# Optimization experiments

Hardware: AMD Instinct MI355X
Metric: run time of the kernel (lower is better)

## Reference

```python
import jax, jax.numpy as jnp
import numpy as np

KS = 3          # deformable kernel size
PAD = 1         # zero padding
N = KS * KS     # sample points per pixel


def conv2d(x, w, b=None, padding=1):
    out = jax.lax.conv_general_dilated(
        x, w, (1, 1), [(padding, padding)] * 2,
        dimension_numbers=('NCHW', 'OIHW', 'NCHW'))
    if b is not None:
        out = out + b[None, :, None, None]
    return out


def setup_inputs() -> dict:
    key = jax.random.key(0)
    k0, k1, k2, k3 = jax.random.split(key, 4)
    B, C, H, W, O = 4, 64, 128, 128, 64
    x = jax.random.normal(k0, (B, C, H, W), jnp.float32)
    # p_conv / m_conv are zero-init in the original; use small random weights
    # so offsets/modulation are non-trivial but sampling stays local.
    w_p = jax.random.normal(k1, (2 * N, C, 3, 3), jnp.float32) * 0.01
    b_p = jnp.zeros((2 * N,), jnp.float32)
    w_m = jax.random.normal(k2, (N, C, 3, 3), jnp.float32) * 0.01
    b_m = jnp.zeros((N,), jnp.float32)
    w_conv = jax.random.normal(k3, (O, C, KS, KS), jnp.float32) / np.sqrt(C * N)
    return {'x': x, 'w_p': w_p, 'b_p': b_p, 'w_m': w_m, 'b_m': b_m, 'w_conv': w_conv}


def reference(x, w_p, b_p, w_m, b_m, w_conv):
    B, C, H, W = x.shape
    offset = conv2d(x, w_p, b_p)              # (B, 2N, H, W): first N rows(x), last N cols(y)
    m = jax.nn.sigmoid(conv2d(x, w_m, b_m))   # (B, N, H, W) modulation
    xp = jnp.pad(x, ((0, 0), (0, 0), (PAD, PAD), (PAD, PAD)))  # zero_padding
    Hp, Wp = H + 2 * PAD, W + 2 * PAD

    # p = p_0 + p_n + offset  (coords in padded image, p_0 starts at 1)
    r = (KS - 1) // 2
    pn_x, pn_y = jnp.meshgrid(jnp.arange(-r, r + 1), jnp.arange(-r, r + 1), indexing='ij')
    pn = jnp.concatenate([pn_x.reshape(-1), pn_y.reshape(-1)]).astype(x.dtype)          # (2N,)
    p0_x, p0_y = jnp.meshgrid(jnp.arange(1, H + 1), jnp.arange(1, W + 1), indexing='ij')
    p0 = jnp.concatenate([jnp.tile(p0_x[None], (N, 1, 1)),
                          jnp.tile(p0_y[None], (N, 1, 1))], 0).astype(x.dtype)           # (2N,H,W)
    p = offset + pn[None, :, None, None] + p0[None]
    p = jnp.moveaxis(p, 1, -1)                # (B,H,W,2N)

    fx = jnp.floor(jax.lax.stop_gradient(p[..., :N]))  # p.detach().floor()
    fy = jnp.floor(jax.lax.stop_gradient(p[..., N:]))
    q_lt_x = jnp.clip(fx, 0, Hp - 1).astype(jnp.int32)
    q_lt_y = jnp.clip(fy, 0, Wp - 1).astype(jnp.int32)
    q_rb_x = jnp.clip(fx + 1, 0, Hp - 1).astype(jnp.int32)
    q_rb_y = jnp.clip(fy + 1, 0, Wp - 1).astype(jnp.int32)
    px = jnp.clip(p[..., :N], 0, Hp - 1)
    py = jnp.clip(p[..., N:], 0, Wp - 1)

    # bilinear kernel weights (same algebra as torch version)
    g_lt = (1 + (q_lt_x - px)) * (1 + (q_lt_y - py))
    g_rb = (1 - (q_rb_x - px)) * (1 - (q_rb_y - py))
    g_lb = (1 + (q_lt_x - px)) * (1 - (q_rb_y - py))
    g_rt = (1 - (q_rb_x - px)) * (1 + (q_lt_y - py))

    xf = xp.reshape(B, C, Hp * Wp)

    def gather(qx, qy):
        idx = (qx * Wp + qy).reshape(B, 1, -1)                      # (B,1,H*W*N)
        return jnp.take_along_axis(xf, idx, axis=2).reshape(B, C, H, W, N)

    x_off = (g_lt[:, None] * gather(q_lt_x, q_lt_y)
             + g_rb[:, None] * gather(q_rb_x, q_rb_y)
             + g_lb[:, None] * gather(q_lt_x, q_rb_y)
             + g_rt[:, None] * gather(q_rb_x, q_lt_y))               # (B,C,H,W,N)

    x_off = x_off * jnp.moveaxis(m, 1, -1)[:, None]                  # modulation (DCNv2)

    # _reshape_x_offset + conv(kernel=ks, stride=ks) == einsum over the N samples
    out = jnp.einsum('bchwk,ock->bohw', x_off,
                     w_conv.reshape(w_conv.shape[0], C, N))
    return out
```

## Files before the change

### kernel.cpp

```cpp
#include <hip/hip_runtime.h>
#include <hip/hip_bf16.h>

#define BB 4
#define CC 64
#define HH 128
#define WW 128
#define OO 64
#define NN 9
#define HW 16384
#define HP 130
#define WP 130

#define WPMB_F  0
#define BPM_OFF 9216
#define WCB_F   9248
#define XT_F    27680
#define PX_OFF  2124832
#define PSZ     589824

typedef __attribute__((ext_vector_type(8))) short s8v;
typedef __attribute__((ext_vector_type(8))) unsigned short u8v;
typedef __attribute__((ext_vector_type(4))) float f4v;

__device__ __forceinline__ unsigned short f2bu(float f) {
    unsigned int b = __float_as_uint(f);
    return (unsigned short)((b + 0x7FFFu + ((b >> 16) & 1u)) >> 16);
}
__device__ __forceinline__ float bu2f(unsigned short u) {
    return __uint_as_float(((unsigned int)u) << 16);
}

__global__ void __launch_bounds__(256) k_pxt(const float* __restrict__ x,
                                             const float* __restrict__ wp,
                                             const float* __restrict__ bp,
                                             const float* __restrict__ wm,
                                             const float* __restrict__ bm,
                                             const float* __restrict__ wcv,
                                             float* __restrict__ ws) {
    __shared__ unsigned short tile[64][66];
    int blk = blockIdx.x;
    int t = threadIdx.x;
    if (blk >= 1024) {
        int tid = (blk - 1024) * 256 + t;
        if (tid < 18432) {
            int r = tid / 576;
            int kk = tid % 576;
            int kt = kk >> 6;
            int c = kk & 63;
            int dy = kt / 3, dx = kt % 3;
            float v = 0.f;
            if (r < 18)       v = wp[((r * 64 + c) * 3 + dy) * 3 + dx];
            else if (r < 27)  v = wm[(((r - 18) * 64 + c) * 3 + dy) * 3 + dx];
            ((unsigned short*)(ws + WPMB_F))[tid] = f2bu(v);
        } else if (tid < 18459) {
            int i = tid - 18432;
            ws[BPM_OFF + i] = (i < 18) ? bp[i] : bm[i - 18];
        } else if (tid >= 20480) {
            int d = tid - 20480;
            int o = d / 576;
            int kk = d % 576;
            int kt = kk >> 6;
            int c = kk & 63;
            ((unsigned short*)(ws + WCB_F))[o * 576 + kk] = f2bu(wcv[(o * 64 + c) * 9 + kt]);
        }
        return;
    }
    int b = blk >> 8;
    int hw0 = (blk & 255) * 64;
    unsigned short* xt = (unsigned short*)(ws + XT_F);
#pragma unroll
    for (int p = 0; p < 16; p++) {
        int c = p * 4 + (t >> 6);
        int i = t & 63;
        tile[c][i] = f2bu(x[((size_t)(b * 64 + c)) * HW + hw0 + i]);
    }
    __syncthreads();
#pragma unroll
    for (int p = 0; p < 16; p++) {
        int i = p * 4 + (t >> 6);
        int c = t & 63;
        xt[((size_t)(b * HW + hw0 + i)) * 64 + c] = tile[c][i];
    }
}

__global__ void __launch_bounds__(256) k_off(const float* __restrict__ ws,
                                             float* __restrict__ wsout) {
    __shared__ unsigned short Awld[2][32 * 72];
    __shared__ unsigned short Bld[2][64 * 72];

    int t = threadIdx.x;
    int lane = t & 63;
    int wid = t >> 6;
    int ln15 = lane & 15;
    int quad = lane >> 4;

    int blk = blockIdx.x;
    int b = blk >> 8;
    int hw0 = (blk & 255) * 64;

    const unsigned short* wpmb = (const unsigned short*)(ws + WPMB_F);
    const unsigned short* xtb = (const unsigned short*)(ws + XT_F) + (size_t)b * HW * 64;
    const float* bpm = ws + BPM_OFF;

    int aq_row = t >> 3, aq_g = t & 7;
    int bq_pix = t & 63, bq_half = t >> 6;
    int ph = (hw0 + bq_pix) >> 7;
    int pw = (hw0 + bq_pix) & 127;

    f4v acc[2];
    acc[0] = (f4v){0.f, 0.f, 0.f, 0.f};
    acc[1] = (f4v){0.f, 0.f, 0.f, 0.f};

    const u8v z = (u8v){0, 0, 0, 0, 0, 0, 0, 0};

    {
        u8v av = *(const u8v*)(wpmb + aq_row * 576 + aq_g * 8);
        int h2 = ph - 1, w2 = pw - 1;
        bool val = ((unsigned)h2 < 128u) && ((unsigned)w2 < 128u);
        u8v e0 = z, e1 = z;
        if (val) {
            const unsigned short* src = xtb + ((size_t)(h2 * 128 + w2)) * 64 + bq_half * 16;
            e0 = *(const u8v*)(src);
            e1 = *(const u8v*)(src + 8);
        }
        *(u8v*)(&Awld[0][aq_row * 72 + aq_g * 8]) = av;
        *(u8v*)(&Bld[0][bq_pix * 72 + bq_half * 16]) = e0;
        *(u8v*)(&Bld[0][bq_pix * 72 + bq_half * 16 + 8]) = e1;
    }
    __syncthreads();

#pragma unroll 1
    for (int kt = 0; kt < 9; kt++) {
        int cur = kt & 1, nxt = cur ^ 1;
        u8v an = z, n0 = z, n1 = z;
        if (kt < 8) {
            int k2 = kt + 1;
            an = *(const u8v*)(wpmb + aq_row * 576 + k2 * 64 + aq_g * 8);
            int dy = k2 / 3, dx = k2 % 3;
            int h2 = ph + dy - 1, w2 = pw + dx - 1;
            bool val = ((unsigned)h2 < 128u) && ((unsigned)w2 < 128u);
            if (val) {
                const unsigned short* src = xtb + ((size_t)(h2 * 128 + w2)) * 64 + bq_half * 16;
                n0 = *(const u8v*)(src);
                n1 = *(const u8v*)(src + 8);
            }
        }
#pragma unroll
        for (int ks = 0; ks < 2; ks++) {
            s8v bf = *(const s8v*)(&Bld[cur][(wid * 16 + ln15) * 72 + ks * 32 + quad * 8]);
#pragma unroll
            for (int mt = 0; mt < 2; mt++) {
                s8v af = *(const s8v*)(&Awld[cur][(mt * 16 + ln15) * 72 + ks * 32 + quad * 8]);
                acc[mt] = __builtin_amdgcn_mfma_f32_16x16x32_bf16(af, bf, acc[mt], 0, 0, 0);
            }
        }
        if (kt < 8) {
            *(u8v*)(&Awld[nxt][aq_row * 72 + aq_g * 8]) = an;
            *(u8v*)(&Bld[nxt][bq_pix * 72 + bq_half * 16]) = n0;
            *(u8v*)(&Bld[nxt][bq_pix * 72 + bq_half * 16 + 8]) = n1;
        }
        __syncthreads();
    }

    int p = hw0 + wid * 16 + ln15;
    int h = p >> 7, w = p & 127;
    float* pxA = wsout + PX_OFF;
    float* pyA = pxA + PSZ;
    float* mmA = pyA + PSZ;
#pragma unroll
    for (int mt = 0; mt < 2; mt++) {
#pragma unroll
        for (int r = 0; r < 4; r++) {
            int oc = mt * 16 + quad * 4 + r;
            if (oc < 27) {
                float v = acc[mt][r] + bpm[oc];
                if (oc < 9) {
                    int ki = oc / 3;
                    pxA[((size_t)b * NN + oc) * HW + p] = v + (float)(ki - 1) + (float)(h + 1);
                } else if (oc < 18) {
                    int k = oc - 9;
                    int kj = k % 3;
                    pyA[((size_t)b * NN + k) * HW + p] = v + (float)(kj - 1) + (float)(w + 1);
                } else {
                    int k = oc - 18;
                    mmA[((size_t)b * NN + k) * HW + p] = 1.f / (1.f + __expf(-v));
                }
            }
        }
    }
}

__global__ void __launch_bounds__(256) k_gemm(const float* __restrict__ ws,
                                              float* __restrict__ out) {
    __shared__ unsigned short Ald[2][64 * 72];
    __shared__ unsigned short Sld[2][64 * 72];

    int t = threadIdx.x;
    int lane = t & 63;
    int wid = t >> 6;
    int ln15 = lane & 15;
    int quad = lane >> 4;

    int blk = blockIdx.x;
    int b = blk >> 8;
    int hw0 = (blk & 255) * 64;

    const unsigned short* wcb = (const unsigned short*)(ws + WCB_F);
    const unsigned short* xtb = (const unsigned short*)(ws + XT_F) + (size_t)b * HW * 64;
    const float* pxA = ws + PX_OFF;
    const float* pyA = pxA + PSZ;
    const float* mmA = pyA + PSZ;

    int p_loc = t >> 2;
    int cq = t & 3;
    int cbase = cq * 16;
    int arow = t >> 2, ag = t & 3;

    f4v acc[4];
#pragma unroll
    for (int mt = 0; mt < 4; mt++) acc[mt] = (f4v){0.f, 0.f, 0.f, 0.f};

    size_t pbase = (size_t)b * NN * HW + (size_t)(hw0 + p_loc);

    auto desc = [&](float px, float py, float mk,
                    float& g0, float& g1, float& g2, float& g3,
                    int& o0, int& o1, int& o2, int& o3) {
        float fx = floorf(px), fy = floorf(py);
        float pxc = fminf(fmaxf(px, 0.f), (float)(HP - 1));
        float pyc = fminf(fmaxf(py, 0.f), (float)(WP - 1));
        int qltx = (int)fminf(fmaxf(fx, 0.f), (float)(HP - 1));
        int qlty = (int)fminf(fmaxf(fy, 0.f), (float)(WP - 1));
        int qrbx = (int)fminf(fmaxf(fx + 1.f, 0.f), (float)(HP - 1));
        int qrby = (int)fminf(fmaxf(fy + 1.f, 0.f), (float)(WP - 1));

        float gltx = 1.f + ((float)qltx - pxc);
        float glty = 1.f + ((float)qlty - pyc);
        float grbx = 1.f - ((float)qrbx - pxc);
        float grby = 1.f - ((float)qrby - pyc);

        bool vlx = (qltx >= 1) && (qltx <= HH);
        bool vly = (qlty >= 1) && (qlty <= WW);
        bool vrx = (qrbx >= 1) && (qrbx <= HH);
        bool vry = (qrby >= 1) && (qrby <= WW);
        g0 = (vlx && vly) ? gltx * glty * mk : 0.f;
        g1 = (vrx && vry) ? grbx * grby * mk : 0.f;
        g2 = (vlx && vry) ? gltx * grby * mk : 0.f;
        g3 = (vrx && vly) ? grbx * glty * mk : 0.f;

        int xlt = min(max(qltx - 1, 0), HH - 1);
        int ylt = min(max(qlty - 1, 0), WW - 1);
        int xrb = min(max(qrbx - 1, 0), HH - 1);
        int yrb = min(max(qrby - 1, 0), WW - 1);
        o0 = (xlt * WW + ylt) * 64 + cbase;
        o1 = (xrb * WW + yrb) * 64 + cbase;
        o2 = (xlt * WW + yrb) * 64 + cbase;
        o3 = (xrb * WW + ylt) * 64 + cbase;
    };

    float pxn, pyn, mkn;
    {
        float px = pxA[pbase], py = pyA[pbase], mk = mmA[pbase];
        pxn = pxA[pbase + HW]; pyn = pyA[pbase + HW]; mkn = mmA[pbase + HW];
        float g0, g1, g2, g3; int o0, o1, o2, o3;
        desc(px, py, mk, g0, g1, g2, g3, o0, o1, o2, o3);
        u8v e0a = *(const u8v*)(xtb + o0), e0b = *(const u8v*)(xtb + o0 + 8);
        u8v e1a = *(const u8v*)(xtb + o1), e1b = *(const u8v*)(xtb + o1 + 8);
        u8v e2a = *(const u8v*)(xtb + o2), e2b = *(const u8v*)(xtb + o2 + 8);
        u8v e3a = *(const u8v*)(xtb + o3), e3b = *(const u8v*)(xtb + o3 + 8);
        u8v a0 = *(const u8v*)(wcb + arow * 576 + ag * 16);
        u8v a1 = *(const u8v*)(wcb + arow * 576 + ag * 16 + 8);
        u8v sva, svb;
#pragma unroll
        for (int j = 0; j < 8; j++) {
            float va = g0 * bu2f(e0a[j]) + g1 * bu2f(e1a[j])
                     + g2 * bu2f(e2a[j]) + g3 * bu2f(e3a[j]);
            float vb = g0 * bu2f(e0b[j]) + g1 * bu2f(e1b[j])
                     + g2 * bu2f(e2b[j]) + g3 * bu2f(e3b[j]);
            sva[j] = f2bu(va);
            svb[j] = f2bu(vb);
        }
        *(u8v*)(&Sld[0][p_loc * 72 + cbase]) = sva;
        *(u8v*)(&Sld[0][p_loc * 72 + cbase + 8]) = svb;
        *(u8v*)(&Ald[0][arow * 72 + ag * 16]) = a0;
        *(u8v*)(&Ald[0][arow * 72 + ag * 16 + 8]) = a1;
    }
    __syncthreads();

#pragma unroll 1
    for (int kt = 0; kt < 9; kt++) {
        int cur = kt & 1, nxt = cur ^ 1;
        float g0 = 0.f, g1 = 0.f, g2 = 0.f, g3 = 0.f;
        u8v e0a, e0b, e1a, e1b, e2a, e2b, e3a, e3b, a0, a1;
        if (kt < 8) {
            int o0, o1, o2, o3;
            desc(pxn, pyn, mkn, g0, g1, g2, g3, o0, o1, o2, o3);
            e0a = *(const u8v*)(xtb + o0); e0b = *(const u8v*)(xtb + o0 + 8);
            e1a = *(const u8v*)(xtb + o1); e1b = *(const u8v*)(xtb + o1 + 8);
            e2a = *(const u8v*)(xtb + o2); e2b = *(const u8v*)(xtb + o2 + 8);
            e3a = *(const u8v*)(xtb + o3); e3b = *(const u8v*)(xtb + o3 + 8);
            a0 = *(const u8v*)(wcb + arow * 576 + (kt + 1) * 64 + ag * 16);
            a1 = *(const u8v*)(wcb + arow * 576 + (kt + 1) * 64 + ag * 16 + 8);
            if (kt < 7) {
                size_t pn = pbase + (size_t)(kt + 2) * HW;
                pxn = pxA[pn]; pyn = pyA[pn]; mkn = mmA[pn];
            }
        }
#pragma unroll
        for (int ks = 0; ks < 2; ks++) {
            s8v bf = *(const s8v*)(&Sld[cur][(wid * 16 + ln15) * 72 + ks * 32 + quad * 8]);
#pragma unroll
            for (int mt = 0; mt < 4; mt++) {
                s8v af = *(const s8v*)(&Ald[cur][(mt * 16 + ln15) * 72 + ks * 32 + quad * 8]);
                acc[mt] = __builtin_amdgcn_mfma_f32_16x16x32_bf16(af, bf, acc[mt], 0, 0, 0);
            }
        }
        if (kt < 8) {
            u8v sva, svb;
#pragma unroll
            for (int j = 0; j < 8; j++) {
                float va = g0 * bu2f(e0a[j]) + g1 * bu2f(e1a[j])
                         + g2 * bu2f(e2a[j]) + g3 * bu2f(e3a[j]);
                float vb = g0 * bu2f(e0b[j]) + g1 * bu2f(e1b[j])
                         + g2 * bu2f(e2b[j]) + g3 * bu2f(e3b[j]);
                sva[j] = f2bu(va);
                svb[j] = f2bu(vb);
            }
            *(u8v*)(&Sld[nxt][p_loc * 72 + cbase]) = sva;
            *(u8v*)(&Sld[nxt][p_loc * 72 + cbase + 8]) = svb;
            *(u8v*)(&Ald[nxt][arow * 72 + ag * 16]) = a0;
            *(u8v*)(&Ald[nxt][arow * 72 + ag * 16 + 8]) = a1;
        }
        __syncthreads();
    }

    int pix = hw0 + wid * 16 + ln15;
    float* ob = out + (size_t)b * (OO * HW) + pix;
#pragma unroll
    for (int mt = 0; mt < 4; mt++) {
#pragma unroll
        for (int r = 0; r < 4; r++) {
            ob[(size_t)(mt * 16 + quad * 4 + r) * HW] = acc[mt][r];
        }
    }
}

extern "C" void kernel_launch(void* const* d_in, const int* in_sizes, int n_in,
                              void* d_out, int out_size, void* d_ws, size_t ws_size,
                              hipStream_t stream) {
    const float* x   = (const float*)d_in[0];
    const float* wp  = (const float*)d_in[1];
    const float* bp  = (const float*)d_in[2];
    const float* wm  = (const float*)d_in[3];
    const float* bm  = (const float*)d_in[4];
    const float* wcv = (const float*)d_in[5];
    float* ws = (float*)d_ws;
    float* out = (float*)d_out;

    hipLaunchKernelGGL(k_pxt, dim3(1248), dim3(256), 0, stream, x, wp, bp, wm, bm, wcv, ws);
    hipLaunchKernelGGL(k_off, dim3(1024), dim3(256), 0, stream, ws, ws);
    hipLaunchKernelGGL(k_gemm, dim3(1024), dim3(256), 0, stream, ws, out);
}
```

Measured before the change: 116.0 us.

## Fuse offset conv and deformable gemm into one kernel via LDS handoff

Merges the offset/modulation MFMA kernel and the deformable-sampling GEMM kernel into a single kernel. Per-block px/py/mask values now stay in shared memory instead of going through global workspace, which removes one launch and the global write/read of those arrays. Weight fragments (offset-conv and main-conv weights) are also read straight from global/L2 into MFMA operands instead of being staged through LDS, which cuts LDS traffic and usage. In exchange, register pressure rises in the fused kernel and the weight loads now sit on the MFMA critical path.

```diff
diff --git a/kernel.cpp b/kernel.cpp
--- a/kernel.cpp
+++ b/kernel.cpp
@@ -15,8 +15,6 @@
 #define BPM_OFF 9216
 #define WCB_F   9248
 #define XT_F    27680
-#define PX_OFF  2124832
-#define PSZ     589824
 
 typedef __attribute__((ext_vector_type(8))) short s8v;
 typedef __attribute__((ext_vector_type(8))) unsigned short u8v;
@@ -83,10 +81,10 @@
     }
 }
 
-__global__ void __launch_bounds__(256) k_off(const float* __restrict__ ws,
-                                             float* __restrict__ wsout) {
-    __shared__ unsigned short Awld[2][32 * 72];
-    __shared__ unsigned short Bld[2][64 * 72];
+__global__ void __launch_bounds__(256) k_main(const float* __restrict__ ws,
+                                              float* __restrict__ out) {
+    __shared__ unsigned short Sld[2][64 * 72];
+    __shared__ float pxmL[3][NN][64];
 
     int t = threadIdx.x;
     int lane = t & 63;
@@ -99,132 +97,107 @@
     int hw0 = (blk & 255) * 64;
 
     const unsigned short* wpmb = (const unsigned short*)(ws + WPMB_F);
+    const unsigned short* wcb = (const unsigned short*)(ws + WCB_F);
     const unsigned short* xtb = (const unsigned short*)(ws + XT_F) + (size_t)b * HW * 64;
     const float* bpm = ws + BPM_OFF;
 
-    int aq_row = t >> 3, aq_g = t & 7;
-    int bq_pix = t & 63, bq_half = t >> 6;
-    int ph = (hw0 + bq_pix) >> 7;
-    int pw = (hw0 + bq_pix) & 127;
-
-    f4v acc[2];
-    acc[0] = (f4v){0.f, 0.f, 0.f, 0.f};
-    acc[1] = (f4v){0.f, 0.f, 0.f, 0.f};
-
     const u8v z = (u8v){0, 0, 0, 0, 0, 0, 0, 0};
 
     {
-        u8v av = *(const u8v*)(wpmb + aq_row * 576 + aq_g * 8);
-        int h2 = ph - 1, w2 = pw - 1;
-        bool val = ((unsigned)h2 < 128u) && ((unsigned)w2 < 128u);
-        u8v e0 = z, e1 = z;
-        if (val) {
-            const unsigned short* src = xtb + ((size_t)(h2 * 128 + w2)) * 64 + bq_half * 16;
-            e0 = *(const u8v*)(src);
-            e1 = *(const u8v*)(src + 8);
-        }
-        *(u8v*)(&Awld[0][aq_row * 72 + aq_g * 8]) = av;
-        *(u8v*)(&Bld[0][bq_pix * 72 + bq_half * 16]) = e0;
-        *(u8v*)(&Bld[0][bq_pix * 72 + bq_half * 16 + 8]) = e1;
-    }
-    __syncthreads();
-
-#pragma unroll 1
-    for (int kt = 0; kt < 9; kt++) {
-        int cur = kt & 1, nxt = cur ^ 1;
-        u8v an = z, n0 = z, n1 = z;
-        if (kt < 8) {
-            int k2 = kt + 1;
-            an = *(const u8v*)(wpmb + aq_row * 576 + k2 * 64 + aq_g * 8);
-            int dy = k2 / 3, dx = k2 % 3;
-            int h2 = ph + dy - 1, w2 = pw + dx - 1;
+        int bq_pix = t & 63, bq_half = t >> 6;
+        int ph = (hw0 + bq_pix) >> 7;
+        int pw = (hw0 + bq_pix) & 127;
+
+        f4v acc[2];
+        acc[0] = (f4v){0.f, 0.f, 0.f, 0.f};
+        acc[1] = (f4v){0.f, 0.f, 0.f, 0.f};
+
+        {
+            int h2 = ph - 1, w2 = pw - 1;
             bool val = ((unsigned)h2 < 128u) && ((unsigned)w2 < 128u);
+            u8v e0 = z, e1 = z;
             if (val) {
                 const unsigned short* src = xtb + ((size_t)(h2 * 128 + w2)) * 64 + bq_half * 16;
-                n0 = *(const u8v*)(src);
-                n1 = *(const u8v*)(src + 8);
-            }
-        }
-#pragma unroll
-        for (int ks = 0; ks < 2; ks++) {
-            s8v bf = *(const s8v*)(&Bld[cur][(wid * 16 + ln15) * 72 + ks * 32 + quad * 8]);
-#pragma unroll
-            for (int mt = 0; mt < 2; mt++) {
-                s8v af = *(const s8v*)(&Awld[cur][(mt * 16 + ln15) * 72 + ks * 32 + quad * 8]);
-                acc[mt] = __builtin_amdgcn_mfma_f32_16x16x32_bf16(af, bf, acc[mt], 0, 0, 0);
-            }
-        }
-        if (kt < 8) {
-            *(u8v*)(&Awld[nxt][aq_row * 72 + aq_g * 8]) = an;
-            *(u8v*)(&Bld[nxt][bq_pix * 72 + bq_half * 16]) = n0;
-            *(u8v*)(&Bld[nxt][bq_pix * 72 + bq_half * 16 + 8]) = n1;
+                e0 = *(const u8v*)(src);
+                e1 = *(const u8v*)(src + 8);
+            }
+            *(u8v*)(&Sld[0][bq_pix * 72 + bq_half * 16]) = e0;
+            *(u8v*)(&Sld[0][bq_pix * 72 + bq_half * 16 + 8]) = e1;
         }
         __syncthreads();
-    }
-
-    int p = hw0 + wid * 16 + ln15;
-    int h = p >> 7, w = p & 127;
-    float* pxA = wsout + PX_OFF;
-    float* pyA = pxA + PSZ;
-    float* mmA = pyA + PSZ;
-#pragma unroll
-    for (int mt = 0; mt < 2; mt++) {
-#pragma unroll
-        for (int r = 0; r < 4; r++) {
-            int oc = mt * 16 + quad * 4 + r;
-            if (oc < 27) {
-                float v = acc[mt][r] + bpm[oc];
-                if (oc < 9) {
-                    int ki = oc / 3;
-                    pxA[((size_t)b * NN + oc) * HW + p] = v + (float)(ki - 1) + (float)(h + 1);
-                } else if (oc < 18) {
-                    int k = oc - 9;
-                    int kj = k % 3;
-                    pyA[((size_t)b * NN + k) * HW + p] = v + (float)(kj - 1) + (float)(w + 1);
-                } else {
-                    int k = oc - 18;
-                    mmA[((size_t)b * NN + k) * HW + p] = 1.f / (1.f + __expf(-v));
+
+#pragma unroll 1
+        for (int kt = 0; kt < 9; kt++) {
+            int cur = kt & 1, nxt = cur ^ 1;
+            u8v n0 = z, n1 = z;
+            if (kt < 8) {
+                int k2 = kt + 1;
+                int dy = k2 / 3, dx = k2 % 3;
+                int h2 = ph + dy - 1, w2 = pw + dx - 1;
+                bool val = ((unsigned)h2 < 128u) && ((unsigned)w2 < 128u);
+                if (val) {
+                    const unsigned short* src = xtb + ((size_t)(h2 * 128 + w2)) * 64 + bq_half * 16;
+                    n0 = *(const u8v*)(src);
+                    n1 = *(const u8v*)(src + 8);
                 }
             }
-        }
-    }
-}
-
-__global__ void __launch_bounds__(256) k_gemm(const float* __restrict__ ws,
-                                              float* __restrict__ out) {
-    __shared__ unsigned short Ald[2][64 * 72];
-    __shared__ unsigned short Sld[2][64 * 72];
-
-    int t = threadIdx.x;
-    int lane = t & 63;
-    int wid = t >> 6;
-    int ln15 = lane & 15;
-    int quad = lane >> 4;
-
-    int blk = blockIdx.x;
-    int b = blk >> 8;
-    int hw0 = (blk & 255) * 64;
-
-    const unsigned short* wcb = (const unsigned short*)(ws + WCB_F);
-    const unsigned short* xtb = (const unsigned short*)(ws + XT_F) + (size_t)b * HW * 64;
-    const float* pxA = ws + PX_OFF;
-    const float* pyA = pxA + PSZ;
-    const float* mmA = pyA + PSZ;
+#pragma unroll
+            for (int ks = 0; ks < 2; ks++) {
+                s8v bf = *(const s8v*)(&Sld[cur][(wid * 16 + ln15) * 72 + ks * 32 + quad * 8]);
+#pragma unroll
+                for (int mt = 0; mt < 2; mt++) {
+                    s8v af = *(const s8v*)(wpmb + (mt * 16 + ln15) * 576 + kt * 64 + ks * 32 + quad * 8);
+                    acc[mt] = __builtin_amdgcn_mfma_f32_16x16x32_bf16(af, bf, acc[mt], 0, 0, 0);
+                }
+            }
+            if (kt < 8) {
+                *(u8v*)(&Sld[nxt][bq_pix * 72 + bq_half * 16]) = n0;
+                *(u8v*)(&Sld[nxt][bq_pix * 72 + bq_half * 16 + 8]) = n1;
+            }
+            __syncthreads();
+        }
+
+        int p = hw0 + wid * 16 + ln15;
+        int h = p >> 7, w = p & 127;
+        int pix = wid * 16 + ln15;
+#pragma unroll
+        for (int mt = 0; mt < 2; mt++) {
+#pragma unroll
+            for (int r = 0; r < 4; r++) {
+                int oc = mt * 16 + quad * 4 + r;
+                if (oc < 27) {
+                    float v = acc[mt][r] + bpm[oc];
+                    if (oc < 9) {
+                        int ki = oc / 3;
+                        pxmL[0][oc][pix] = v + (float)(ki - 1) + (float)(h + 1);
+                    } else if (oc < 18) {
+                        int k = oc - 9;
+                        int kj = k % 3;
+                        pxmL[1][k][pix] = v + (float)(kj - 1) + (float)(w + 1);
+                    } else {
+                        int k = oc - 18;
+                        pxmL[2][k][pix] = 1.f / (1.f + __expf(-v));
+                    }
+                }
+            }
+        }
+    }
+    __syncthreads();
 
     int p_loc = t >> 2;
     int cq = t & 3;
     int cbase = cq * 16;
-    int arow = t >> 2, ag = t & 3;
 
     f4v acc[4];
 #pragma unroll
     for (int mt = 0; mt < 4; mt++) acc[mt] = (f4v){0.f, 0.f, 0.f, 0.f};
 
-    size_t pbase = (size_t)b * NN * HW + (size_t)(hw0 + p_loc);
-
-    auto desc = [&](float px, float py, float mk,
+    auto desc = [&](int kt,
                     float& g0, float& g1, float& g2, float& g3,
                     int& o0, int& o1, int& o2, int& o3) {
+        float px = pxmL[0][kt][p_loc];
+        float py = pxmL[1][kt][p_loc];
+        float mk = pxmL[2][kt][p_loc];
         float fx = floorf(px), fy = floorf(py);
         float pxc = fminf(fmaxf(px, 0.f), (float)(HP - 1));
         float pyc = fminf(fmaxf(py, 0.f), (float)(WP - 1));
@@ -257,18 +230,13 @@
         o3 = (xrb * WW + ylt) * 64 + cbase;
     };
 
-    float pxn, pyn, mkn;
     {
-        float px = pxA[pbase], py = pyA[pbase], mk = mmA[pbase];
-        pxn = pxA[pbase + HW]; pyn = pyA[pbase + HW]; mkn = mmA[pbase + HW];
         float g0, g1, g2, g3; int o0, o1, o2, o3;
-        desc(px, py, mk, g0, g1, g2, g3, o0, o1, o2, o3);
+        desc(0, g0, g1, g2, g3, o0, o1, o2, o3);
         u8v e0a = *(const u8v*)(xtb + o0), e0b = *(const u8v*)(xtb + o0 + 8);
         u8v e1a = *(const u8v*)(xtb + o1), e1b = *(const u8v*)(xtb + o1 + 8);
         u8v e2a = *(const u8v*)(xtb + o2), e2b = *(const u8v*)(xtb + o2 + 8);
         u8v e3a = *(const u8v*)(xtb + o3), e3b = *(const u8v*)(xtb + o3 + 8);
-        u8v a0 = *(const u8v*)(wcb + arow * 576 + ag * 16);
-        u8v a1 = *(const u8v*)(wcb + arow * 576 + ag * 16 + 8);
         u8v sva, svb;
 #pragma unroll
         for (int j = 0; j < 8; j++) {
@@ -281,8 +249,6 @@
         }
         *(u8v*)(&Sld[0][p_loc * 72 + cbase]) = sva;
         *(u8v*)(&Sld[0][p_loc * 72 + cbase + 8]) = svb;
-        *(u8v*)(&Ald[0][arow * 72 + ag * 16]) = a0;
-        *(u8v*)(&Ald[0][arow * 72 + ag * 16 + 8]) = a1;
     }
     __syncthreads();
 
@@ -290,27 +256,21 @@
     for (int kt = 0; kt < 9; kt++) {
         int cur = kt & 1, nxt = cur ^ 1;
         float g0 = 0.f, g1 = 0.f, g2 = 0.f, g3 = 0.f;
-        u8v e0a, e0b, e1a, e1b, e2a, e2b, e3a, e3b, a0, a1;
+        u8v e0a, e0b, e1a, e1b, e2a, e2b, e3a, e3b;
         if (kt < 8) {
             int o0, o1, o2, o3;
-            desc(pxn, pyn, mkn, g0, g1, g2, g3, o0, o1, o2, o3);
+            desc(kt + 1, g0, g1, g2, g3, o0, o1, o2, o3);
             e0a = *(const u8v*)(xtb + o0); e0b = *(const u8v*)(xtb + o0 + 8);
             e1a = *(const u8v*)(xtb + o1); e1b = *(const u8v*)(xtb + o1 + 8);
             e2a = *(const u8v*)(xtb + o2); e2b = *(const u8v*)(xtb + o2 + 8);
             e3a = *(const u8v*)(xtb + o3); e3b = *(const u8v*)(xtb + o3 + 8);
-            a0 = *(const u8v*)(wcb + arow * 576 + (kt + 1) * 64 + ag * 16);
-            a1 = *(const u8v*)(wcb + arow * 576 + (kt + 1) * 64 + ag * 16 + 8);
-            if (kt < 7) {
-                size_t pn = pbase + (size_t)(kt + 2) * HW;
-                pxn = pxA[pn]; pyn = pyA[pn]; mkn = mmA[pn];
-            }
         }
 #pragma unroll
         for (int ks = 0; ks < 2; ks++) {
             s8v bf = *(const s8v*)(&Sld[cur][(wid * 16 + ln15) * 72 + ks * 32 + quad * 8]);
 #pragma unroll
             for (int mt = 0; mt < 4; mt++) {
-                s8v af = *(const s8v*)(&Ald[cur][(mt * 16 + ln15) * 72 + ks * 32 + quad * 8]);
+                s8v af = *(const s8v*)(wcb + (mt * 16 + ln15) * 576 + kt * 64 + ks * 32 + quad * 8);
                 acc[mt] = __builtin_amdgcn_mfma_f32_16x16x32_bf16(af, bf, acc[mt], 0, 0, 0);
             }
         }
@@ -327,8 +287,6 @@
             }
             *(u8v*)(&Sld[nxt][p_loc * 72 + cbase]) = sva;
             *(u8v*)(&Sld[nxt][p_loc * 72 + cbase + 8]) = svb;
-            *(u8v*)(&Ald[nxt][arow * 72 + ag * 16]) = a0;
-            *(u8v*)(&Ald[nxt][arow * 72 + ag * 16 + 8]) = a1;
         }
         __syncthreads();
     }
@@ -357,6 +315,5 @@
     float* out = (float*)d_out;
 
     hipLaunchKernelGGL(k_pxt, dim3(1248), dim3(256), 0, stream, x, wp, bp, wm, bm, wcv, ws);
-    hipLaunchKernelGGL(k_off, dim3(1024), dim3(256), 0, stream, ws, ws);
-    hipLaunchKernelGGL(k_gemm, dim3(1024), dim3(256), 0, stream, ws, out);
-}
+    hipLaunchKernelGGL(k_main, dim3(1024), dim3(256), 0, stream, ws, out);
+}
```

Measured after the change: 149.9 us. +29.3%, slower.
